# Kernel optimization log

Measured on AMD Instinct MI355X. Metric: run time of the kernel, lower is better.

Reference implementation:

```python
import jax, jax.numpy as jnp
import numpy as np

# ---- Cayley-Dickson octonion multiplication tables (SIGN_TABLE, WEIGHT_IDX) ----
def _cd_conj(a):
    n = a.shape[0]
    if n == 1:
        return a
    h = n // 2
    return np.concatenate([_cd_conj(a[:h]), -a[h:]])

def _cd_mul(a, b):
    n = a.shape[0]
    if n == 1:
        return a * b
    h = n // 2
    a1, a2 = a[:h], a[h:]
    c1, c2 = b[:h], b[h:]
    # (a1,a2)(c1,c2) = (a1 c1 - conj(c2) a2, c2 a1 + a2 conj(c1))
    return np.concatenate([_cd_mul(a1, c1) - _cd_mul(_cd_conj(c2), a2),
                           _cd_mul(c2, a1) + _cd_mul(a2, _cd_conj(c1))])

def _octonion_tables():
    signs = np.zeros((8, 8), dtype=np.float32)
    widx = np.zeros((8, 8), dtype=np.int32)
    for i in range(8):
        for j in range(8):
            ei = np.zeros(8); ei[i] = 1.0
            ej = np.zeros(8); ej[j] = 1.0
            p = _cd_mul(ei, ej)
            k = int(np.argmax(np.abs(p)))  # == i ^ j
            signs[i, j] = np.sign(p[k])
            widx[i, j] = k
    return jnp.asarray(signs), jnp.asarray(widx)

SIGNS, WIDX = _octonion_tables()


def ternary_ste(W):
    # BitNet-style per-matrix ternary quantization with straight-through estimator.
    s = jnp.mean(jnp.abs(W), axis=(-2, -1), keepdims=True) + 1e-8
    Wq = jnp.clip(jnp.round(W / s), -1.0, 1.0) * s
    return W + jax.lax.stop_gradient(Wq - W)


def oct_linear(x, W):
    # x: [B,T,C] split into 8 parts of C/8; out_i = sum_j sign[i,j] * x_j @ Wq[i^j]
    B, T, C = x.shape
    c8 = C // 8
    x8 = x.reshape(B, T, 8, c8)
    Wq = ternary_ste(W)          # [8, c8, c8]
    Wg = Wq[WIDX]                # [8, 8, c8, c8]
    out = jnp.einsum('ij,btjc,ijcd->btid', SIGNS, x8, Wg)
    return out.reshape(B, T, C)


def apply_rope(q, freqs_cos, freqs_sin):
    # q: [B,T,H,D]; complex pairs are (q[...,2k], q[...,2k+1])
    qe, qo = q[..., 0::2], q[..., 1::2]
    cos = freqs_cos[None, :, None, :]
    sin = freqs_sin[None, :, None, :]
    oe = qe * cos - qo * sin
    oo = qe * sin + qo * cos
    return jnp.stack([oe, oo], axis=-1).reshape(q.shape)


def setup_inputs() -> dict:
    key = jax.random.key(0)
    ks = jax.random.split(key, 8)
    B, T, C, H = 4, 1024, 2048, 16
    D = C // H           # 128
    c8 = C // 8          # 256
    x = jax.random.normal(ks[0], (B, T, C), dtype=jnp.float32)
    # RoPE tables (theta = 10000)
    inv = 1.0 / (10000.0 ** (jnp.arange(0, D, 2, dtype=jnp.float32) / D))
    ang = jnp.arange(T, dtype=jnp.float32)[:, None] * inv[None, :]   # [T, D/2]
    freqs_cos = jnp.cos(ang)
    freqs_sin = jnp.sin(ang)
    wq = jax.random.normal(ks[1], (8, c8, c8), dtype=jnp.float32) * 0.02
    wk = jax.random.normal(ks[2], (8, c8, c8), dtype=jnp.float32) * 0.02
    wv = jax.random.normal(ks[3], (8, c8, c8), dtype=jnp.float32) * 0.02
    wo = jax.random.normal(ks[4], (8, c8, c8), dtype=jnp.float32) * 0.02
    mixer_W = jax.random.normal(ks[5], (8, D, D), dtype=jnp.float32) * 0.02
    mixer_beta = jnp.ones((D,), dtype=jnp.float32) * 0.1
    return {"x": x, "freqs_cos": freqs_cos, "freqs_sin": freqs_sin,
            "wq": wq, "wk": wk, "wv": wv, "wo": wo,
            "mixer_W": mixer_W, "mixer_beta": mixer_beta}


def reference(x, freqs_cos, freqs_sin, wq, wk, wv, wo, mixer_W, mixer_beta):
    B, T, C = x.shape
    H = 16
    D = C // H
    q = oct_linear(x, wq).reshape(B, T, H, D)
    k = oct_linear(x, wk).reshape(B, T, H, D)
    v = oct_linear(x, wv).reshape(B, T, H, D)
    q = apply_rope(q, freqs_cos, freqs_sin)
    k = apply_rope(k, freqs_cos, freqs_sin)
    q, k, v = (jnp.transpose(t, (0, 2, 1, 3)) for t in (q, k, v))  # [B,H,T,D]
    # causal SDPA
    scale = 1.0 / jnp.sqrt(jnp.asarray(D, dtype=q.dtype))
    scores = jnp.einsum('bhqd,bhkd->bhqk', q, k) * scale
    mask = jnp.tril(jnp.ones((T, T), dtype=bool))
    scores = jnp.where(mask, scores, jnp.asarray(-1e30, dtype=scores.dtype))
    probs = jax.nn.softmax(scores, axis=-1)
    y = jnp.einsum('bhqk,bhkd->bhqd', probs, v)  # [B,H,T,D]
    # octonion head mixing per group of 8 heads
    G = H // 8
    y8 = y.reshape(B, G, 8, T, D)
    Wg = mixer_W[WIDX]  # [8,8,D,D]
    y8 = jnp.einsum('ij,bgjtd,ijde->bgite', SIGNS, y8, Wg) * mixer_beta
    y = y8.reshape(B, H, T, D)
    y = jnp.transpose(y, (0, 2, 1, 3)).reshape(B, T, C)
    return oct_linear(y, wo)
```

## Files before the change

### kernel.cpp

```cpp
#include <hip/hip_runtime.h>
#include <math.h>

#define CDIM 2048
#define QKVW 6144

typedef __bf16 bf16x8 __attribute__((ext_vector_type(8)));
typedef __bf16 bf16x4 __attribute__((ext_vector_type(4)));
typedef float  f32x4  __attribute__((ext_vector_type(4)));
typedef float  f32x16 __attribute__((ext_vector_type(16)));

__device__ __constant__ float SIGNS_c[64] = {
  1,  1,  1,  1,  1,  1,  1,  1,
  1, -1,  1, -1,  1, -1, -1,  1,
  1, -1, -1,  1,  1,  1, -1, -1,
  1,  1, -1, -1,  1, -1,  1, -1,
  1, -1, -1, -1, -1,  1,  1,  1,
  1,  1, -1,  1, -1, -1, -1,  1,
  1,  1,  1, -1, -1,  1, -1, -1,
  1, -1,  1,  1, -1, -1,  1, -1
};

__device__ __forceinline__ void load_lds16(const void* g, void* lp) {
  __builtin_amdgcn_global_load_lds(
      (const __attribute__((address_space(1))) unsigned int*)g,
      (__attribute__((address_space(3))) unsigned int*)lp, 16, 0, 0);
}

__device__ __forceinline__ void wg_barrier() {
  asm volatile("" ::: "memory");
  __builtin_amdgcn_s_barrier();
  asm volatile("" ::: "memory");
}

__device__ __forceinline__ unsigned pack2(float a, float b) {
  union { __bf16 h[2]; unsigned u; } x;
  x.h[0] = (__bf16)a; x.h[1] = (__bf16)b; return x.u;
}

__global__ __launch_bounds__(256)
void cast_scale(const float* __restrict__ x, __bf16* __restrict__ xb,
                const float* __restrict__ wq, const float* __restrict__ wk,
                const float* __restrict__ wv, const float* __restrict__ wo,
                double* __restrict__ part) {
  __shared__ double red[256];
  if (blockIdx.x < 8192) {
    int i = blockIdx.x * 256 + threadIdx.x;
    float4 v = *(const float4*)(x + (size_t)i * 4);
    bf16x4 o;
    o[0] = (__bf16)v.x; o[1] = (__bf16)v.y; o[2] = (__bf16)v.z; o[3] = (__bf16)v.w;
    *(bf16x4*)(xb + (size_t)i * 4) = o;
    return;
  }
  int bid = blockIdx.x - 8192;
  int which = bid >> 6, m = (bid >> 3) & 7, seg = bid & 7;
  const float* W = (which == 0) ? wq : (which == 1) ? wk : (which == 2) ? wv : wo;
  const float4* w4 = (const float4*)(W + (m << 16) + seg * 8192);
  double acc = 0.0;
  #pragma unroll
  for (int i = 0; i < 8; ++i) {
    float4 v = w4[threadIdx.x + i * 256];
    acc += (double)fabsf(v.x) + (double)fabsf(v.y) +
           (double)fabsf(v.z) + (double)fabsf(v.w);
  }
  red[threadIdx.x] = acc;
  __syncthreads();
  for (int s = 128; s > 0; s >>= 1) {
    if (threadIdx.x < s) red[threadIdx.x] += red[threadIdx.x + s];
    __syncthreads();
  }
  if (threadIdx.x == 0) part[bid] = red[0];
}

__global__ void scale_fin(const double* __restrict__ part, double* __restrict__ s8,
                          double* __restrict__ rs8) {
  int t = threadIdx.x;
  if (t < 32) {
    double a = 0.0;
    #pragma unroll
    for (int i = 0; i < 8; ++i) a += part[t * 8 + i];
    double s = a / 65536.0 + 1e-8;
    s8[t] = s;
    rs8[t] = 1.0 / s;
  }
}

__global__ void build_oct3(const float* __restrict__ wq, const float* __restrict__ wk,
                           const float* __restrict__ wv, const double* __restrict__ s8,
                           const double* __restrict__ rs8, __bf16* __restrict__ MT) {
  int z = blockIdx.y;
  const float* W = (z == 0) ? wq : (z == 1) ? wk : wv;
  const double* sp = s8 + z * 8;
  const double* rp = rs8 + z * 8;
  __bf16* out = MT + (size_t)z * 4194304;
  int idx = blockIdx.x * 256 + threadIdx.x;
  int row = idx & 2047, col = idx >> 11;
  int i = col >> 8, d = col & 255, j = row >> 8, c = row & 255;
  int m = i ^ j;
  double q = rint((double)W[(m << 16) + (c << 8) + d] * rp[m]);
  q = fmin(fmax(q, -1.0), 1.0);
  out[idx] = (__bf16)(SIGNS_c[i * 8 + j] * (float)(q * sp[m]));
}

__global__ void build_oct_T(const float* __restrict__ W, const double* __restrict__ s8,
                            const double* __restrict__ rs8, __bf16* __restrict__ MT) {
  int idx = blockIdx.x * 256 + threadIdx.x;
  int row = idx & 2047, col = idx >> 11;
  int i = col >> 8, d = col & 255, j = row >> 8, c = row & 255;
  int m = i ^ j;
  double q = rint((double)W[(m << 16) + (c << 8) + d] * rs8[m]);
  q = fmin(fmax(q, -1.0), 1.0);
  MT[idx] = (__bf16)(SIGNS_c[i * 8 + j] * (float)(q * s8[m]));
}

__global__ void build_mix_plain(const float* __restrict__ Wm, const float* __restrict__ beta,
                                __bf16* __restrict__ M) {
  int idx = blockIdx.x * 256 + threadIdx.x;
  int kl = idx & 1023, kpl = idx >> 10;
  int j = kpl >> 7, dd = kpl & 127;
  int i = kl >> 7, e = kl & 127;
  M[idx] = (__bf16)(SIGNS_c[i * 8 + j] * Wm[((i ^ j) << 14) + (dd << 7) + e] * beta[e]);
}

__global__ __launch_bounds__(512, 2)
void gemm_qkv8(const __bf16* __restrict__ A, const __bf16* __restrict__ BT,
               const float* __restrict__ fc, const float* __restrict__ fs,
               __bf16* __restrict__ C) {
  __shared__ __align__(16) char smem[131072];
  int tid = threadIdx.x;
  int w = tid >> 6, l = tid & 63, hi = l >> 4, lo = l & 15;
  int wm = w >> 2, wn = w & 3;
  int lin = blockIdx.x;
  int xcd = lin & 7, idx = lin >> 3;
  int cy = xcd >> 2, cx = xcd & 3;
  int iby = idx >> 3, ibx = idx & 7;
  int bm = (cy * 8 + iby) * 256;
  int bn = (cx * 8 + ibx) * 192;
  const char* Ab = (const char*)A + (size_t)bm * 4096;
  const char* Bb = (const char*)BT + (size_t)bn * 4096;

  int sw = (((lo & 1) << 2) + hi) ^ (lo >> 1);

  int se_r[2], se_g[2], se_rb[2];
  #pragma unroll
  for (int q = 0; q < 2; ++q) {
    int e = q * 512 + tid;
    int lr = e >> 3, sl = e & 7;
    int x = sl ^ (lr & 7);
    se_r[q] = lr * 2 + (x >> 2);
    se_g[q] = x & 3;
    se_rb[q] = se_r[q] < 192 ? se_r[q] : 191;
  }
  int dstoff[2] = { (0 * 512 + w * 64) * 16, (1 * 512 + w * 64) * 16 };

  f32x4 acc[8][3];
  #pragma unroll
  for (int m = 0; m < 8; ++m)
    #pragma unroll
    for (int n = 0; n < 3; ++n) acc[m][n] = (f32x4){0.f, 0.f, 0.f, 0.f};
  bf16x8 bfr[3];

  #define STG(MAT, TT, KH) do {                                                  \
    char* dst_ = smem + ((TT) & 1) * 65536 + (MAT) * 32768 + (KH) * 16384;       \
    const char* gb_ = (MAT) ? Bb : Ab;                                           \
    _Pragma("unroll")                                                            \
    for (int q = 0; q < 2; ++q) {                                                \
      int r_ = (MAT) ? se_rb[q] : se_r[q];                                       \
      load_lds16(gb_ + (size_t)r_ * 4096 + ((TT) * 64 + (KH) * 32) * 2 + se_g[q] * 16, \
                 dst_ + dstoff[q]);                                              \
    }                                                                            \
  } while (0)

  #define QUAD(TT, KH, MSUB, READB) do {                                         \
    const char* ar_ = smem + ((TT) & 1) * 65536 + (KH) * 16384;                  \
    const char* br_ = ar_ + 32768;                                               \
    if (READB) {                                                                 \
      _Pragma("unroll")                                                          \
      for (int n = 0; n < 3; ++n)                                                \
        bfr[n] = *(const bf16x8*)(br_ + (wn * 24 + n * 8 + (lo >> 1)) * 128 + sw * 16); \
    }                                                                            \
    bf16x8 afr[4];                                                               \
    _Pragma("unroll")                                                            \
    for (int m = 0; m < 4; ++m)                                                  \
      afr[m] = *(const bf16x8*)(ar_ + (wm * 64 + (MSUB) * 32 + m * 8 + (lo >> 1)) * 128 + sw * 16); \
    __builtin_amdgcn_s_setprio(1);                                               \
    _Pragma("unroll")                                                            \
    for (int m = 0; m < 4; ++m)                                                  \
      _Pragma("unroll")                                                          \
      for (int n = 0; n < 3; ++n)                                                \
        acc[(MSUB) * 4 + m][n] =                                                 \
            __builtin_amdgcn_mfma_f32_16x16x32_bf16(afr[m], bfr[n], acc[(MSUB) * 4 + m][n], 0, 0, 0); \
    __builtin_amdgcn_s_setprio(0);                                               \
  } while (0)

  #define LGK0() asm volatile("s_waitcnt lgkmcnt(0)" ::: "memory")
  #define VMW8() asm volatile("s_waitcnt vmcnt(8)" ::: "memory")
  #define VMW4() asm volatile("s_waitcnt vmcnt(4)" ::: "memory")
  #define VMW0() asm volatile("s_waitcnt vmcnt(0)" ::: "memory")

  STG(0, 0, 0); STG(1, 0, 0);
  STG(0, 0, 1); STG(1, 0, 1);
  STG(0, 1, 0); STG(1, 1, 0);
  VMW8();
  wg_barrier();

  #define GITER(T0, LAST) do {                                                   \
     STG(0, (T0) + 1, 1); QUAD((T0), 0, 0, 1); wg_barrier();            \
     STG(1, (T0) + 1, 1); QUAD((T0), 0, 1, 0); LGK0(); VMW8(); wg_barrier(); \
     if (!(LAST)) { STG(0, (T0) + 2, 0); } QUAD((T0), 1, 0, 1); wg_barrier(); \
     if (!(LAST)) { STG(1, (T0) + 2, 0); } QUAD((T0), 1, 1, 0); LGK0(); \
              if (LAST) { VMW4(); } else { VMW8(); } wg_barrier();               \
     if (!(LAST)) { STG(0, (T0) + 2, 1); } QUAD((T0) + 1, 0, 0, 1); wg_barrier(); \
     if (!(LAST)) { STG(1, (T0) + 2, 1); } QUAD((T0) + 1, 0, 1, 0); LGK0(); \
              if (LAST) { VMW0(); } else { VMW8(); } wg_barrier();               \
     if (!(LAST)) { STG(0, (T0) + 3, 0); } QUAD((T0) + 1, 1, 0, 1); wg_barrier(); \
     if (!(LAST)) { STG(1, (T0) + 3, 0); } QUAD((T0) + 1, 1, 1, 0);     \
              if (!(LAST)) { LGK0(); VMW8(); wg_barrier(); }                     \
  } while (0)

  for (int i = 0; i < 15; ++i) GITER(2 * i, false);
  GITER(30, true);

  #undef GITER
  #undef STG
  #undef QUAD
  #undef VMW8
  #undef VMW4
  #undef LGK0
  #undef VMW0

  #pragma unroll
  for (int mm = 0; mm < 8; ++mm)
    #pragma unroll
    for (int n = 0; n < 3; ++n) {
      int col = bn + wn * 48 + n * 16 + lo;
      int isqk = (col < 4096);
      int p = (col & 127) >> 1;
      int evenl = ((col & 1) == 0);
      #pragma unroll
      for (int r = 0; r < 4; ++r) {
        int row = bm + wm * 128 + mm * 16 + hi * 4 + r;
        float v = acc[mm][n][r];
        float other = __shfl_xor(v, 1, 64);
        if (isqk) {
          int t = row & 1023;
          float c = fc[t * 64 + p];
          float s = fs[t * 64 + p];
          v = evenl ? (v * c - other * s) : (other * s + v * c);
        }
        C[(size_t)row * QKVW + col] = (__bf16)v;
      }
    }
}

__global__ __launch_bounds__(512, 2)
void gemm_fin8(const __bf16* __restrict__ A, const __bf16* __restrict__ BT,
               float* __restrict__ C) {
  __shared__ __align__(16) char smem[98304];
  int tid = threadIdx.x;
  int w = tid >> 6, l = tid & 63, hi = l >> 4, lo = l & 15;
  int wm = w >> 2, wn = w & 3;
  int lin = blockIdx.x;
  int xcd = lin & 7, idx = lin >> 3;
  int cy = xcd >> 1, cx = xcd & 1;
  int iby = idx >> 2, ibx = idx & 3;
  int bm = (cy * 8 + iby) * 128;
  int bn = (cx * 4 + ibx) * 256;
  const char* Ab = (const char*)A + (size_t)bm * 12288;
  const char* Bb = (const char*)BT + (size_t)bn * 4096;

  int sw = (((lo & 1) << 2) + hi) ^ (lo >> 1);

  int se_r[2], se_g[2];
  #pragma unroll
  for (int q = 0; q < 2; ++q) {
    int e = q * 512 + tid;
    int lr = e >> 3, sl = e & 7;
    int x = sl ^ (lr & 7);
    se_r[q] = lr * 2 + (x >> 2);
    se_g[q] = x & 3;
  }
  int dstoff[2] = { (0 * 512 + w * 64) * 16, (1 * 512 + w * 64) * 16 };

  f32x4 acc[4][4];
  #pragma unroll
  for (int m = 0; m < 4; ++m)
    #pragma unroll
    for (int n = 0; n < 4; ++n) acc[m][n] = (f32x4){0.f, 0.f, 0.f, 0.f};
  bf16x8 bfr[4];

  #define STG(MAT, TT, KH) do {                                                  \
    char* ab_ = smem + ((TT) & 1) * 49152;                                       \
    char* dst_ = (MAT) ? (ab_ + 16384 + (KH) * 16384) : (ab_ + (KH) * 8192);     \
    const char* gb_ = (MAT) ? Bb : Ab;                                           \
    size_t ld_ = (MAT) ? 4096 : 12288;                                           \
    int nq_ = (MAT) ? 2 : 1;                                                     \
    _Pragma("unroll")                                                            \
    for (int q = 0; q < 2; ++q)                                                  \
      if (q < nq_)                                                               \
        load_lds16(gb_ + (size_t)se_r[q] * ld_ + ((TT) * 64 + (KH) * 32) * 2 + se_g[q] * 16, \
                   dst_ + dstoff[q]);                                            \
  } while (0)

  #define QUAD(TT, KH, MSUB, READB) do {                                         \
    const char* ab_ = smem + ((TT) & 1) * 49152;                                 \
    const char* ar_ = ab_ + (KH) * 8192;                                         \
    const char* br_ = ab_ + 16384 + (KH) * 16384;                                \
    if (READB) {                                                                 \
      _Pragma("unroll")                                                          \
      for (int n = 0; n < 4; ++n)                                                \
        bfr[n] = *(const bf16x8*)(br_ + (wn * 32 + n * 8 + (lo >> 1)) * 128 + sw * 16); \
    }                                                                            \
    bf16x8 afr[2];                                                               \
    _Pragma("unroll")                                                            \
    for (int m = 0; m < 2; ++m)                                                  \
      afr[m] = *(const bf16x8*)(ar_ + (wm * 32 + (MSUB) * 16 + m * 8 + (lo >> 1)) * 128 + sw * 16); \
    __builtin_amdgcn_s_setprio(1);                                               \
    _Pragma("unroll")                                                            \
    for (int m = 0; m < 2; ++m)                                                  \
      _Pragma("unroll")                                                          \
      for (int n = 0; n < 4; ++n)                                                \
        acc[(MSUB) * 2 + m][n] =                                                 \
            __builtin_amdgcn_mfma_f32_16x16x32_bf16(afr[m], bfr[n], acc[(MSUB) * 2 + m][n], 0, 0, 0); \
    __builtin_amdgcn_s_setprio(0);                                               \
  } while (0)

  #define LGK0() asm volatile("s_waitcnt lgkmcnt(0)" ::: "memory")
  #define VMW6() asm volatile("s_waitcnt vmcnt(6)" ::: "memory")
  #define VMW3() asm volatile("s_waitcnt vmcnt(3)" ::: "memory")
  #define VMW0() asm volatile("s_waitcnt vmcnt(0)" ::: "memory")

  STG(0, 0, 0); STG(1, 0, 0);
  STG(0, 0, 1); STG(1, 0, 1);
  STG(0, 1, 0); STG(1, 1, 0);
  VMW6();
  wg_barrier();

  #define GITER(T0, LAST) do {                                                   \
     STG(0, (T0) + 1, 1); QUAD((T0), 0, 0, 1); wg_barrier();            \
     STG(1, (T0) + 1, 1); QUAD((T0), 0, 1, 0); LGK0(); VMW6(); wg_barrier(); \
     if (!(LAST)) { STG(0, (T0) + 2, 0); } QUAD((T0), 1, 0, 1); wg_barrier(); \
     if (!(LAST)) { STG(1, (T0) + 2, 0); } QUAD((T0), 1, 1, 0); LGK0(); \
              if (LAST) { VMW3(); } else { VMW6(); } wg_barrier();               \
     if (!(LAST)) { STG(0, (T0) + 2, 1); } QUAD((T0) + 1, 0, 0, 1); wg_barrier(); \
     if (!(LAST)) { STG(1, (T0) + 2, 1); } QUAD((T0) + 1, 0, 1, 0); LGK0(); \
              if (LAST) { VMW0(); } else { VMW6(); } wg_barrier();               \
     if (!(LAST)) { STG(0, (T0) + 3, 0); } QUAD((T0) + 1, 1, 0, 1); wg_barrier(); \
     if (!(LAST)) { STG(1, (T0) + 3, 0); } QUAD((T0) + 1, 1, 1, 0);     \
              if (!(LAST)) { LGK0(); VMW6(); wg_barrier(); }                     \
  } while (0)

  for (int i = 0; i < 15; ++i) GITER(2 * i, false);
  GITER(30, true);

  #undef GITER
  #undef STG
  #undef QUAD
  #undef VMW6
  #undef VMW3
  #undef LGK0
  #undef VMW0

  #pragma unroll
  for (int mm = 0; mm < 4; ++mm)
    #pragma unroll
    for (int n = 0; n < 4; ++n)
      #pragma unroll
      for (int r = 0; r < 4; ++r) {
        int row = bm + wm * 64 + mm * 16 + hi * 4 + r;
        int col = bn + wn * 64 + n * 16 + lo;
        C[(size_t)row * 2048 + col] = acc[mm][n][r];
      }
}

template<int BN, int NBY, int NBX, int CBY, int CBX, int KLEN, int LDA, int OUT_BF16>
__global__ __launch_bounds__(512, 2)
void gemm_ps(const __bf16* __restrict__ A, const __bf16* __restrict__ BT,
             void* __restrict__ Cout, int az, int cz, int ldc) {
  constexpr int FN = BN / 64;
  constexpr int LB = (BN > 128) ? 2 : 1;
  constexpr int VC = 2 + LB;
  constexpr int BUFSZ = 16384 + 8192 * LB;
  constexpr int CGX = NBX / CBX;
  static_assert((NBY / CBY) * CGX == 8, "chunk grid must be 8 XCDs");
  __shared__ __align__(16) char smem[2 * BUFSZ];
  int tid = threadIdx.x;
  int w = tid >> 6, l = tid & 63, hi = l >> 4, lo = l & 15;
  int wm = w >> 2, wn = w & 3;
  int lin = blockIdx.x;
  int xcd = lin & 7, idx = lin >> 3;
  int cy = xcd / CGX, cx = xcd % CGX;
  int iby = idx / CBX, ibx = idx % CBX;
  int bm = (cy * CBY + iby) * 256;
  int bn = (cx * CBX + ibx) * BN;
  const char* Ab = (const char*)(A + (size_t)blockIdx.y * az) + (size_t)bm * LDA * 2;
  const char* Bb = (const char*)BT + (size_t)bn * KLEN * 2;

  int sw = (((lo & 1) << 2) + hi) ^ (lo >> 1);
  int base_a = (wm * 64 + (lo >> 1)) * 128 + sw * 16;
  int base_b = 16384 + (wn * (BN / 8) + (lo >> 1)) * 128 + sw * 16;

  int se_r[2], se_g[2];
  #pragma unroll
  for (int q = 0; q < 2; ++q) {
    int e = q * 512 + tid;
    int lr = e >> 3, sl = e & 7;
    int x = sl ^ (lr & 7);
    se_r[q] = lr * 2 + (x >> 2);
    se_g[q] = x & 3;
  }
  int dstoff[2] = { (0 * 512 + w * 64) * 16, (1 * 512 + w * 64) * 16 };

  f32x4 acc[8][FN];
  #pragma unroll
  for (int m = 0; m < 8; ++m)
    #pragma unroll
    for (int n = 0; n < FN; ++n) acc[m][n] = (f32x4){0.f, 0.f, 0.f, 0.f};

  #define STAGE(BUFI, K0) do {                                                   \
    char* As_ = smem + (BUFI) * BUFSZ;                                           \
    char* Bs_ = As_ + 16384;                                                     \
    _Pragma("unroll")                                                            \
    for (int q = 0; q < 2; ++q)                                                  \
      load_lds16(Ab + (size_t)se_r[q] * (LDA * 2) + (size_t)(K0) * 2 + se_g[q] * 16, \
                 As_ + dstoff[q]);                                               \
    _Pragma("unroll")                                                            \
    for (int q = 0; q < LB; ++q)                                                 \
      load_lds16(Bb + (size_t)se_r[q] * (KLEN * 2) + (size_t)(K0) * 2 + se_g[q] * 16, \
                 Bs_ + dstoff[q]);                                               \
  } while (0)

  #define WAITVC() do {                                                \
    if constexpr (VC == 4) asm volatile("s_waitcnt vmcnt(4)" ::: "memory"); \
    else                   asm volatile("s_waitcnt vmcnt(3)" ::: "memory"); \
  } while (0)

  constexpr int NT = KLEN / 32;
  STAGE(0, 0);
  STAGE(1, 32);
  WAITVC();
  wg_barrier();

  for (int t = 0; t < NT; ++t) {
    char* buf = smem + (t & 1) * BUFSZ;
    bf16x8 bfr[FN], afr[8];
    #pragma unroll
    for (int n = 0; n < FN; ++n) bfr[n] = *(const bf16x8*)(buf + base_b + n * 1024);
    #pragma unroll
    for (int m = 0; m < 8; ++m) afr[m] = *(const bf16x8*)(buf + base_a + m * 1024);
    __builtin_amdgcn_s_setprio(1);
    #pragma unroll
    for (int m = 0; m < 4; ++m)
      #pragma unroll
      for (int n = 0; n < FN; ++n)
        acc[m][n] = __builtin_amdgcn_mfma_f32_16x16x32_bf16(afr[m], bfr[n], acc[m][n], 0, 0, 0);
    __builtin_amdgcn_s_setprio(0);
    asm volatile("s_waitcnt lgkmcnt(0)" ::: "memory");
    wg_barrier();

    if (t + 2 < NT) STAGE(t & 1, (t + 2) * 32);
    __builtin_amdgcn_s_setprio(1);
    #pragma unroll
    for (int m = 4; m < 8; ++m)
      #pragma unroll
      for (int n = 0; n < FN; ++n)
        acc[m][n] = __builtin_amdgcn_mfma_f32_16x16x32_bf16(afr[m], bfr[n], acc[m][n], 0, 0, 0);
    __builtin_amdgcn_s_setprio(0);
    if (t + 2 < NT) { WAITVC(); }
    else            { asm volatile("s_waitcnt vmcnt(0)" ::: "memory"); }
    wg_barrier();
  }
  #undef STAGE
  #undef WAITVC

  #pragma unroll
  for (int m = 0; m < 8; ++m)
    #pragma unroll
    for (int n = 0; n < FN; ++n)
      #pragma unroll
      for (int r = 0; r < 4; ++r) {
        int row = bm + wm * 128 + m * 16 + hi * 4 + r;
        int col = bn + wn * (BN / 4) + n * 16 + lo;
        if (OUT_BF16)
          ((__bf16*)Cout)[(size_t)blockIdx.y * cz + (size_t)row * ldc + col] = (__bf16)acc[m][n][r];
        else
          ((float*)Cout)[(size_t)blockIdx.y * cz + (size_t)row * ldc + col] = acc[m][n][r];
      }
}

__global__ __launch_bounds__(256)
void transpose_v(const __bf16* __restrict__ QKV, __bf16* __restrict__ VT) {
  __shared__ __bf16 tile[64][136];
  int tid = threadIdx.x;
  int tt = blockIdx.x;
  int bh = blockIdx.y;
  int b = bh >> 4, h = bh & 15;
  int t0 = tt * 64;
  #pragma unroll
  for (int q = 0; q < 4; ++q) {
    int i = q * 256 + tid;
    int tr = i >> 4, u = i & 15;
    bf16x8 v = *(const bf16x8*)(QKV + (size_t)(b * 1024 + t0 + tr) * QKVW + 4096 + h * 128 + u * 8);
    *(bf16x8*)&tile[tr][u * 8] = v;
  }
  __syncthreads();
  #pragma unroll
  for (int q = 0; q < 4; ++q) {
    int i = q * 256 + tid;
    int d = i >> 3, tu = i & 7;
    bf16x8 o;
    #pragma unroll
    for (int jj = 0; jj < 8; ++jj) o[jj] = tile[tu * 8 + jj][d];
    *(bf16x8*)(VT + ((size_t)bh * 128 + d) * 1024 + t0 + tu * 8) = o;
  }
}

__global__ __launch_bounds__(256, 2)
void attn_mfma2(__bf16* __restrict__ QKV, const __bf16* __restrict__ VT) {
  __shared__ __align__(16) char smem[65536];
  int tid = threadIdx.x;
  int w = tid >> 6, l = tid & 63;
  int lo = l & 31, hv = l >> 5;
  int wgid = blockIdx.x;
  int xcd = wgid & 7, idx = wgid >> 3;
  int s = idx & 7, j = s >> 1, odd = s & 1, hi5 = idx >> 5;
  int base = hi5 ? 7 - j : j;
  int qt = odd ? 7 - base : base;
  int bh = xcd * 8 + (idx >> 3);
  int b = bh >> 4, h = bh & 15;
  int qb = qt * 128;
  int wq0 = qb + w * 32;
  int qrow = wq0 + lo;
  const __bf16* qp = QKV + (size_t)(b * 1024 + qrow) * QKVW + h * 128;
  bf16x8 qf[8];
  #pragma unroll
  for (int c = 0; c < 8; ++c) qf[c] = *(const bf16x8*)(qp + c * 16 + hv * 8);

  f32x16 o[4];
  #pragma unroll
  for (int n = 0; n < 4; ++n)
    #pragma unroll
    for (int r = 0; r < 16; ++r) o[n][r] = 0.f;
  float mrun = -1e30f, lrun = 0.f;
  const float SCL = 0.08838834764831845f * 1.4426950408889634f;
  int src0 = lo, src1 = 32 + lo;
  int nt = 2 * qt + 2;

  #define ASTAGE(BUF, KT) do {                                                   \
    _Pragma("unroll")                                                            \
    for (int i = 0; i < 4; ++i) {                                                \
      int e = i * 256 + tid;                                                     \
      int row = e >> 4, g = e & 15;                                              \
      int gs = g ^ (row & 7);                                                    \
      const char* src = (const char*)QKV +                                       \
          ((size_t)(b * 1024 + (KT) * 64 + row) * QKVW + 2048 + h * 128) * 2 + gs * 16; \
      load_lds16(src, smem + (BUF) * 16384 + (i * 256 + w * 64) * 16);           \
    }                                                                            \
    _Pragma("unroll")                                                            \
    for (int i = 0; i < 4; ++i) {                                                \
      int e = i * 256 + tid;                                                     \
      int row = e >> 3, g = e & 7;                                               \
      int gs = g ^ (row & 7);                                                    \
      const char* src = (const char*)VT +                                        \
          ((size_t)(bh * 128 + row) * 1024 + (KT) * 64) * 2 + gs * 16;           \
      load_lds16(src, smem + 32768 + (BUF) * 16384 + (i * 256 + w * 64) * 16);   \
    }                                                                            \
  } while (0)

  ASTAGE(0, 0);
  asm volatile("s_waitcnt vmcnt(0)" ::: "memory");
  wg_barrier();

  for (int kt = 0; kt < nt; ++kt) {
    int cur = kt & 1;
    if (kt + 1 < nt) ASTAGE(cur ^ 1, kt + 1);
    int k0 = kt * 64;
    char* Ks  = smem + cur * 16384;
    char* VTs = smem + 32768 + cur * 16384;

    if (k0 <= wq0 + 31) {
      f32x16 sT[2];
      #pragma unroll
      for (int kk = 0; kk < 2; ++kk) {
        #pragma unroll
        for (int r = 0; r < 16; ++r) sT[kk][r] = 0.f;
        #pragma unroll
        for (int c = 0; c < 8; ++c) {
          bf16x8 kf = *(const bf16x8*)(Ks + (kk * 32 + lo) * 256 + (((2 * c + hv) ^ (lo & 7)) * 16));
          sT[kk] = __builtin_amdgcn_mfma_f32_32x32x16_bf16(kf, qf[c], sT[kk], 0, 0, 0);
        }
      }
      bool diag = (k0 + 63 > wq0);
      float pv[2][16];
      #pragma unroll
      for (int kk = 0; kk < 2; ++kk)
        #pragma unroll
        for (int r = 0; r < 16; ++r) {
          float v = sT[kk][r] * SCL;
          if (diag) {
            int kg = k0 + kk * 32 + (r & 3) + 8 * (r >> 2) + 4 * hv;
            if (kg > qrow) v = -1e30f;
          }
          pv[kk][r] = v;
        }
      float mx = pv[0][0];
      #pragma unroll
      for (int kk = 0; kk < 2; ++kk)
        #pragma unroll
        for (int r = 0; r < 16; ++r) mx = fmaxf(mx, pv[kk][r]);
      mx = fmaxf(mx, __shfl_xor(mx, 32, 64));
      if (!__all(mx <= mrun + 8.f)) {
        float mnew = fmaxf(mrun, mx);
        float fac = exp2f(mrun - mnew);
        lrun *= fac;
        #pragma unroll
        for (int n = 0; n < 4; ++n)
          #pragma unroll
          for (int r = 0; r < 16; ++r) o[n][r] *= fac;
        mrun = mnew;
      }
      float rs = 0.f;
      #pragma unroll
      for (int kk = 0; kk < 2; ++kk)
        #pragma unroll
        for (int r = 0; r < 16; ++r) {
          float p = exp2f(pv[kk][r] - mrun);
          pv[kk][r] = p;
          rs += p;
        }
      rs += __shfl_xor(rs, 32, 64);
      lrun += rs;

      unsigned pk[2][4][2];
      #pragma unroll
      for (int kk = 0; kk < 2; ++kk)
        #pragma unroll
        for (int m = 0; m < 4; ++m)
          #pragma unroll
          for (int u = 0; u < 2; ++u)
            pk[kk][m][u] = pack2(pv[kk][m * 4 + 2 * u], pv[kk][m * 4 + 2 * u + 1]);

      #pragma unroll
      for (int kk = 0; kk < 2; ++kk) {
        #pragma unroll
        for (int s2 = 0; s2 < 2; ++s2) {
          unsigned a0 = __shfl(pk[kk][2 * s2][0], src0, 64);
          unsigned b0 = __shfl(pk[kk][2 * s2 + 1][0], src0, 64);
          unsigned a1 = __shfl(pk[kk][2 * s2][1], src0, 64);
          unsigned b1 = __shfl(pk[kk][2 * s2 + 1][1], src0, 64);
          unsigned a2 = __shfl(pk[kk][2 * s2][0], src1, 64);
          unsigned b2 = __shfl(pk[kk][2 * s2 + 1][0], src1, 64);
          unsigned a3 = __shfl(pk[kk][2 * s2][1], src1, 64);
          unsigned b3 = __shfl(pk[kk][2 * s2 + 1][1], src1, 64);
          union { unsigned u[4]; bf16x8 v; } pb;
          pb.u[0] = hv ? b0 : a0;
          pb.u[1] = hv ? b1 : a1;
          pb.u[2] = hv ? b2 : a2;
          pb.u[3] = hv ? b3 : a3;
          int ks16 = 2 * kk + s2;
          #pragma unroll
          for (int n = 0; n < 4; ++n) {
            bf16x8 vf = *(const bf16x8*)(VTs + (n * 32 + lo) * 128 +
                                         (((2 * ks16 + hv) ^ (lo & 7)) * 16));
            o[n] = __builtin_amdgcn_mfma_f32_32x32x16_bf16(vf, pb.v, o[n], 0, 0, 0);
          }
        }
      }
    }
    asm volatile("s_waitcnt vmcnt(0)" ::: "memory");
    wg_barrier();
  }
  #undef ASTAGE

  float inv = 1.f / lrun;
  __bf16* op = QKV + (size_t)(b * 1024 + qrow) * QKVW + h * 128;
  #pragma unroll
  for (int n = 0; n < 4; ++n)
    #pragma unroll
    for (int m4 = 0; m4 < 4; ++m4) {
      bf16x4 ov;
      #pragma unroll
      for (int jj = 0; jj < 4; ++jj) ov[jj] = (__bf16)(o[n][m4 * 4 + jj] * inv);
      *(bf16x4*)(op + n * 32 + 8 * m4 + 4 * hv) = ov;
    }
}

extern "C" void kernel_launch(void* const* d_in, const int* in_sizes, int n_in,
                              void* d_out, int out_size, void* d_ws, size_t ws_size,
                              hipStream_t stream) {
  const float* x    = (const float*)d_in[0];
  const float* fc   = (const float*)d_in[1];
  const float* fs   = (const float*)d_in[2];
  const float* wq   = (const float*)d_in[3];
  const float* wk   = (const float*)d_in[4];
  const float* wv   = (const float*)d_in[5];
  const float* wo   = (const float*)d_in[6];
  const float* wm   = (const float*)d_in[7];
  const float* beta = (const float*)d_in[8];

  char* wsb = (char*)d_ws;
  __bf16* xb      = (__bf16*)(wsb);
  __bf16* MTqkv   = (__bf16*)(wsb + 16777216L);
  __bf16* QKV     = (__bf16*)(wsb + 41943040L);
  __bf16* VTb     = (__bf16*)(wsb + 92274688L);
  double* s8      = (double*)(wsb + 109051904L);
  double* part    = (double*)(wsb + 109052160L);
  double* rs8     = (double*)(wsb + 109054208L);
  __bf16* MTwo    = (__bf16*)(wsb);
  __bf16* BTfused = (__bf16*)(wsb + 8388608L);
  __bf16* MTmixP  = MTqkv;

  dim3 blk(256);

  cast_scale<<<8448, blk, 0, stream>>>(x, xb, wq, wk, wv, wo, part);
  scale_fin<<<1, dim3(64), 0, stream>>>(part, s8, rs8);
  build_oct3<<<dim3(16384, 3), blk, 0, stream>>>(wq, wk, wv, s8, rs8, MTqkv);

  gemm_qkv8<<<512, dim3(512), 0, stream>>>(xb, MTqkv, fc, fs, QKV);

  build_oct_T<<<16384, blk, 0, stream>>>(wo, s8 + 24, rs8 + 24, MTwo);
  build_mix_plain<<<4096, blk, 0, stream>>>(wm, beta, MTmixP);
  gemm_ps<128, 8, 8, 2, 4, 1024, 2048, 1>
      <<<dim3(64, 2), dim3(512), 0, stream>>>(MTwo, MTmixP, BTfused, 1024, 1024, 2048);

  transpose_v<<<dim3(16, 64), blk, 0, stream>>>(QKV, VTb);

  attn_mfma2<<<dim3(512), blk, 0, stream>>>(QKV, VTb);

  gemm_fin8<<<256, dim3(512), 0, stream>>>(QKV, BTfused, (float*)d_out);
}
```

Before: 321.0 us.

## Move RoPE out of QKV GEMM epilogue into fused rope+V-transpose kernel

Removes the RoPE rotation (shuffle plus per-element cos/sin loads) from the QKV GEMM epilogue, so the GEMM writes raw bf16. A new kernel applies RoPE in place with vectorized 16-byte loads of q/k and float4 cos/sin, sharing a launch with the V transpose. The wo and mixer weight build kernels are also merged into one launch to save a launch. The trade is an extra read and write pass over the Q and K parts of the QKV buffer, plus double rounding to bf16 before and after the rotation.

```diff
diff --git a/kernel.cpp b/kernel.cpp
--- a/kernel.cpp
+++ b/kernel.cpp
@@ -101,29 +101,29 @@
   out[idx] = (__bf16)(SIGNS_c[i * 8 + j] * (float)(q * sp[m]));
 }
 
-__global__ void build_oct_T(const float* __restrict__ W, const double* __restrict__ s8,
-                            const double* __restrict__ rs8, __bf16* __restrict__ MT) {
-  int idx = blockIdx.x * 256 + threadIdx.x;
-  int row = idx & 2047, col = idx >> 11;
-  int i = col >> 8, d = col & 255, j = row >> 8, c = row & 255;
-  int m = i ^ j;
-  double q = rint((double)W[(m << 16) + (c << 8) + d] * rs8[m]);
-  q = fmin(fmax(q, -1.0), 1.0);
-  MT[idx] = (__bf16)(SIGNS_c[i * 8 + j] * (float)(q * s8[m]));
-}
-
-__global__ void build_mix_plain(const float* __restrict__ Wm, const float* __restrict__ beta,
-                                __bf16* __restrict__ M) {
-  int idx = blockIdx.x * 256 + threadIdx.x;
+__global__ void build_wo_mix(const float* __restrict__ W, const double* __restrict__ s8,
+                             const double* __restrict__ rs8, __bf16* __restrict__ MT,
+                             const float* __restrict__ Wm, const float* __restrict__ beta,
+                             __bf16* __restrict__ Mmix) {
+  if (blockIdx.x < 16384) {
+    int idx = blockIdx.x * 256 + threadIdx.x;
+    int row = idx & 2047, col = idx >> 11;
+    int i = col >> 8, d = col & 255, j = row >> 8, c = row & 255;
+    int m = i ^ j;
+    double q = rint((double)W[(m << 16) + (c << 8) + d] * rs8[m]);
+    q = fmin(fmax(q, -1.0), 1.0);
+    MT[idx] = (__bf16)(SIGNS_c[i * 8 + j] * (float)(q * s8[m]));
+    return;
+  }
+  int idx = (blockIdx.x - 16384) * 256 + threadIdx.x;
   int kl = idx & 1023, kpl = idx >> 10;
   int j = kpl >> 7, dd = kpl & 127;
   int i = kl >> 7, e = kl & 127;
-  M[idx] = (__bf16)(SIGNS_c[i * 8 + j] * Wm[((i ^ j) << 14) + (dd << 7) + e] * beta[e]);
+  Mmix[idx] = (__bf16)(SIGNS_c[i * 8 + j] * Wm[((i ^ j) << 14) + (dd << 7) + e] * beta[e]);
 }
 
 __global__ __launch_bounds__(512, 2)
 void gemm_qkv8(const __bf16* __restrict__ A, const __bf16* __restrict__ BT,
-               const float* __restrict__ fc, const float* __restrict__ fs,
                __bf16* __restrict__ C) {
   __shared__ __align__(16) char smem[131072];
   int tid = threadIdx.x;
@@ -231,25 +231,13 @@
   #pragma unroll
   for (int mm = 0; mm < 8; ++mm)
     #pragma unroll
-    for (int n = 0; n < 3; ++n) {
-      int col = bn + wn * 48 + n * 16 + lo;
-      int isqk = (col < 4096);
-      int p = (col & 127) >> 1;
-      int evenl = ((col & 1) == 0);
+    for (int n = 0; n < 3; ++n)
       #pragma unroll
       for (int r = 0; r < 4; ++r) {
         int row = bm + wm * 128 + mm * 16 + hi * 4 + r;
-        float v = acc[mm][n][r];
-        float other = __shfl_xor(v, 1, 64);
-        if (isqk) {
-          int t = row & 1023;
-          float c = fc[t * 64 + p];
-          float s = fs[t * 64 + p];
-          v = evenl ? (v * c - other * s) : (other * s + v * c);
-        }
-        C[(size_t)row * QKVW + col] = (__bf16)v;
+        int col = bn + wn * 48 + n * 16 + lo;
+        C[(size_t)row * QKVW + col] = (__bf16)acc[mm][n][r];
       }
-    }
 }
 
 __global__ __launch_bounds__(512, 2)
@@ -488,11 +476,40 @@
 }
 
 __global__ __launch_bounds__(256)
-void transpose_v(const __bf16* __restrict__ QKV, __bf16* __restrict__ VT) {
+void rope_transv(__bf16* __restrict__ QKV, const float* __restrict__ fc,
+                 const float* __restrict__ fs, __bf16* __restrict__ VT) {
   __shared__ __bf16 tile[64][136];
   int tid = threadIdx.x;
-  int tt = blockIdx.x;
-  int bh = blockIdx.y;
+  if (blockIdx.x < 4096) {
+    int idx = blockIdx.x * 256 + tid;
+    int pg = idx & 15;
+    int h = (idx >> 4) & 15;
+    int n = idx >> 8;
+    int t = n & 1023;
+    float4 c4 = *(const float4*)(fc + t * 64 + pg * 4);
+    float4 s4 = *(const float4*)(fs + t * 64 + pg * 4);
+    float c[4] = {c4.x, c4.y, c4.z, c4.w};
+    float s[4] = {s4.x, s4.y, s4.z, s4.w};
+    size_t ofs = (size_t)n * QKVW + h * 128 + pg * 8;
+    bf16x8 q = *(bf16x8*)(QKV + ofs);
+    bf16x8 k = *(bf16x8*)(QKV + 2048 + ofs);
+    bf16x8 oq, ok;
+    #pragma unroll
+    for (int j = 0; j < 4; ++j) {
+      float x = (float)q[2 * j], y = (float)q[2 * j + 1];
+      oq[2 * j]     = (__bf16)(x * c[j] - y * s[j]);
+      oq[2 * j + 1] = (__bf16)(x * s[j] + y * c[j]);
+      float u = (float)k[2 * j], vv = (float)k[2 * j + 1];
+      ok[2 * j]     = (__bf16)(u * c[j] - vv * s[j]);
+      ok[2 * j + 1] = (__bf16)(u * s[j] + vv * c[j]);
+    }
+    *(bf16x8*)(QKV + ofs) = oq;
+    *(bf16x8*)(QKV + 2048 + ofs) = ok;
+    return;
+  }
+  int bid = blockIdx.x - 4096;
+  int tt = bid & 15;
+  int bh = bid >> 4;
   int b = bh >> 4, h = bh & 15;
   int t0 = tt * 64;
   #pragma unroll
@@ -715,14 +732,13 @@
   scale_fin<<<1, dim3(64), 0, stream>>>(part, s8, rs8);
   build_oct3<<<dim3(16384, 3), blk, 0, stream>>>(wq, wk, wv, s8, rs8, MTqkv);
 
-  gemm_qkv8<<<512, dim3(512), 0, stream>>>(xb, MTqkv, fc, fs, QKV);
-
-  build_oct_T<<<16384, blk, 0, stream>>>(wo, s8 + 24, rs8 + 24, MTwo);
-  build_mix_plain<<<4096, blk, 0, stream>>>(wm, beta, MTmixP);
+  gemm_qkv8<<<512, dim3(512), 0, stream>>>(xb, MTqkv, QKV);
+
+  build_wo_mix<<<20480, blk, 0, stream>>>(wo, s8 + 24, rs8 + 24, MTwo, wm, beta, MTmixP);
   gemm_ps<128, 8, 8, 2, 4, 1024, 2048, 1>
       <<<dim3(64, 2), dim3(512), 0, stream>>>(MTwo, MTmixP, BTfused, 1024, 1024, 2048);
 
-  transpose_v<<<dim3(16, 64), blk, 0, stream>>>(QKV, VTb);
+  rope_transv<<<5120, blk, 0, stream>>>(QKV, fc, fs, VTb);
 
   attn_mfma2<<<dim3(512), blk, 0, stream>>>(QKV, VTb);
 
```

Measured after the change: 303.6 us. 1.06x faster.
